# Optimization experiments

Hardware: AMD Instinct MI355X
Metric: run time of the kernel (lower is better)

Reference implementation:

```python
import jax, jax.numpy as jnp
import numpy as np

OUT = 7   # output_size
SR = 2    # sampling_ratio


def _roi_align(feat_bhwc, rois, batch_idx, sx, sy):
    """RoIAlign (torchvision semantics, aligned=False) with per-axis spatial scale.
    feat_bhwc: [B,H,W,C]; rois: [K,4] (x1,y1,x2,y2) in padded-image coords;
    batch_idx: [K] int32; returns [K,C,OUT,OUT]."""
    B, H, W, C = feat_bhwc.shape
    K = rois.shape[0]
    x1 = rois[:, 0] * sx
    y1 = rois[:, 1] * sy
    x2 = rois[:, 2] * sx
    y2 = rois[:, 3] * sy
    bw = jnp.maximum(x2 - x1, 1.0) / OUT   # bin width  [K]
    bh = jnp.maximum(y2 - y1, 1.0) / OUT   # bin height [K]
    # sample position j in [0, OUT*SR): offset (j+0.5)/SR bins from roi start
    g = (jnp.arange(OUT * SR, dtype=feat_bhwc.dtype) + 0.5) / SR
    ys = y1[:, None] + g[None, :] * bh[:, None]   # [K, P] with P = OUT*SR
    xs = x1[:, None] + g[None, :] * bw[:, None]   # [K, P]
    Y = ys[:, :, None]                            # [K,P,1]
    X = xs[:, None, :]                            # [K,1,P]
    valid = (Y >= -1.0) & (Y <= H) & (X >= -1.0) & (X <= W)  # [K,P,P]
    Yc = jnp.clip(Y, 0.0, H - 1)
    Xc = jnp.clip(X, 0.0, W - 1)
    y0f = jnp.floor(Yc)
    x0f = jnp.floor(Xc)
    ly = Yc - y0f
    lx = Xc - x0f
    hy = 1.0 - ly
    hx = 1.0 - lx
    y0i = y0f.astype(jnp.int32)
    x0i = x0f.astype(jnp.int32)
    y1i = jnp.minimum(y0i + 1, H - 1)
    x1i = jnp.minimum(x0i + 1, W - 1)
    b = batch_idx[:, None, None]                  # [K,1,1]

    def gat(yi, xi):
        # broadcasts indices to [K,P,P]; gathers [K,P,P,C]
        return feat_bhwc[b, yi, xi]

    out = ((hy * hx)[..., None] * gat(y0i, x0i)
           + (hy * lx)[..., None] * gat(y0i, x1i)
           + (ly * hx)[..., None] * gat(y1i, x0i)
           + (ly * lx)[..., None] * gat(y1i, x1i))
    out = out * valid[..., None].astype(out.dtype)
    # average SRxSR samples per output bin
    out = out.reshape(K, OUT, SR, OUT, SR, C).mean(axis=(2, 4))
    return out.transpose(0, 3, 1, 2)  # [K,C,OUT,OUT]


def reference(x0, x1, x2, boxes, ratio, offset, shape):
    B, C0, H0, W0 = x0.shape
    # bilinear upsample (half-pixel centers == torch align_corners=False) and concat
    up1 = jax.image.resize(x1, (B, x1.shape[1], H0, W0), method='bilinear')
    up2 = jax.image.resize(x2, (B, x2.shape[1], H0, W0), method='bilinear')
    feat = jnp.concatenate([x0, up1, up2], axis=1)      # [B, 3*C, H0, W0]
    feat_bhwc = feat.transpose(0, 2, 3, 1)
    # map boxes from original-image coords to padded/resized coords
    rH, rW = ratio[:, 0], ratio[:, 1]
    top, left = offset[:, 0], offset[:, 1]
    mul = jnp.stack([rW, rH, rW, rH], axis=-1)[:, None, :]   # [B,1,4]
    add = jnp.stack([left, top, left, top], axis=-1)[:, None, :]
    rois = (boxes * mul + add).reshape(-1, 4)                # [K,4]
    N = boxes.shape[1]
    batch_idx = jnp.repeat(jnp.arange(B, dtype=jnp.int32), N)
    # per-axis spatial scale from the first meta (as in the torch code)
    padded_h = jnp.floor(shape[0, 0] * rH[0] + 2.0 * top[0])
    padded_w = jnp.floor(shape[0, 1] * rW[0] + 2.0 * left[0])
    sx = W0 / padded_w
    sy = H0 / padded_h
    return _roi_align(feat_bhwc, rois, batch_idx, sx, sy)   # [B*N, 3*C, 7, 7]


def setup_inputs():
    key = jax.random.key(0)
    k = jax.random.split(key, 5)
    B, C, N = 2, 256, 128
    IH, IW = 800.0, 1216.0  # original image size; stride-8 top level -> 100x152
    x0 = jax.random.normal(k[0], (B, C, 100, 152), jnp.float32)
    x1 = jax.random.normal(k[1], (B, C, 50, 76), jnp.float32)
    x2 = jax.random.normal(k[2], (B, C, 25, 38), jnp.float32)
    xy = jax.random.uniform(k[3], (B, N, 2)) * jnp.array([IW - 64.0, IH - 64.0], jnp.float32)
    wh = 16.0 + jax.random.uniform(k[4], (B, N, 2)) * 200.0
    boxes = jnp.concatenate([xy, jnp.minimum(xy + wh, jnp.array([IW, IH], jnp.float32))], axis=-1)
    ratio = jnp.ones((B, 2), jnp.float32)
    offset = jnp.zeros((B, 2), jnp.float32)
    shape = jnp.tile(jnp.array([[IH, IW]], jnp.float32), (B, 1))
    return dict(x0=x0, x1=x1, x2=x2, boxes=boxes, ratio=ratio, offset=offset, shape=shape)
```

## Files before the change

### kernel.cpp

```cpp
#include <hip/hip_runtime.h>
#include <hip/hip_bf16.h>

constexpr int B  = 2;
constexpr int C  = 256;
constexpr int H0 = 100, W0 = 152;
constexpr int H1 = 50,  W1 = 76;
constexpr int H2 = 25,  W2 = 38;
constexpr int N  = 128;
constexpr int K  = B * N;
constexpr int CT = 3 * C;
constexpr int OUTS = 7;

#define DEV __device__ __forceinline__

DEV float ldbf(const __hip_bfloat16* p) { return __bfloat162float(*p); }

DEV void st4bf(__hip_bfloat16* p, float a, float b, float c, float d) {
  union { __hip_bfloat16 h[4]; uint2 u; } pk;
  pk.h[0] = __float2bfloat16(a); pk.h[1] = __float2bfloat16(b);
  pk.h[2] = __float2bfloat16(c); pk.h[3] = __float2bfloat16(d);
  *reinterpret_cast<uint2*>(p) = pk.u;
}

__global__ __launch_bounds__(256) void fuse_kernel(
    const float* __restrict__ x0, const float* __restrict__ x1,
    const float* __restrict__ x2, __hip_bfloat16* __restrict__ feat) {
  __shared__ float buf[64 * 153];
  const int blk  = blockIdx.x;
  const int tile = blk % 12;
  const int by   = blk / 12;
  const int y    = by % H0;
  const int b    = by / H0;
  const int t    = threadIdx.x;
  const int level = tile >> 2;
  const int c0l   = (tile & 3) * 64;

  __hip_bfloat16* const orow =
      feat + (((size_t)b * H0 + y) * W0) * CT + tile * 64;

  if (level == 0) {
    const float* src = x0 + (((size_t)b * C + c0l) * H0 + y) * W0;
    for (int i = 0; i < 10; ++i) {
      const int lin = i * 256 + t;
      if (lin < 2432) {
        const int cl = lin / 38, xq = lin % 38;
        const float4 v =
            *reinterpret_cast<const float4*>(src + (size_t)cl * (H0 * W0) + xq * 4);
        float* d = &buf[cl * 153 + xq * 4];
        d[0] = v.x; d[1] = v.y; d[2] = v.z; d[3] = v.w;
      }
    }
    __syncthreads();
    for (int i = 0; i < 10; ++i) {
      const int lin = i * 256 + t;
      if (lin < 2432) {
        const int x = lin >> 4, cq = lin & 15;
        st4bf(orow + (size_t)x * CT + cq * 4,
              buf[(cq * 4 + 0) * 153 + x], buf[(cq * 4 + 1) * 153 + x],
              buf[(cq * 4 + 2) * 153 + x], buf[(cq * 4 + 3) * 153 + x]);
      }
    }
  } else if (level == 1) {
    const float fy = fminf(fmaxf(y * 0.5f - 0.25f, 0.f), (float)(H1 - 1));
    const int   y0i = (int)fy;
    const float ly  = fy - (float)y0i;
    const int   y1i = min(y0i + 1, H1 - 1);
    const int rstep = (y1i - y0i) * W1;
    const float* s0 = x1 + (((size_t)b * C + c0l) * H1 + y0i) * W1;
    for (int i = 0; i < 5; ++i) {
      const int lin = i * 256 + t;
      if (lin < 1216) {
        const int cl = lin / 19, xq = lin % 19;
        const float* p = s0 + (size_t)cl * (H1 * W1) + xq * 4;
        const float4 v0 = *reinterpret_cast<const float4*>(p);
        const float4 v1 = *reinterpret_cast<const float4*>(p + rstep);
        float* d = &buf[cl * 81 + xq * 4];
        d[0] = v0.x + ly * (v1.x - v0.x);
        d[1] = v0.y + ly * (v1.y - v0.y);
        d[2] = v0.z + ly * (v1.z - v0.z);
        d[3] = v0.w + ly * (v1.w - v0.w);
      }
    }
    __syncthreads();
    for (int i = 0; i < 10; ++i) {
      const int lin = i * 256 + t;
      if (lin < 2432) {
        const int x = lin >> 4, cq = lin & 15;
        const float fx = fminf(fmaxf(x * 0.5f - 0.25f, 0.f), (float)(W1 - 1));
        const int   x0i = (int)fx;
        const float lx  = fx - (float)x0i;
        const int   x1i = min(x0i + 1, W1 - 1);
        const float* r = &buf[cq * 4 * 81];
        float v[4];
        #pragma unroll
        for (int j = 0; j < 4; ++j) {
          const float a = r[j * 81 + x0i], bb = r[j * 81 + x1i];
          v[j] = a + lx * (bb - a);
        }
        st4bf(orow + (size_t)x * CT + cq * 4, v[0], v[1], v[2], v[3]);
      }
    }
  } else {
    const float fy = fminf(fmaxf(y * 0.25f - 0.375f, 0.f), (float)(H2 - 1));
    const int   y0i = (int)fy;
    const float ly  = fy - (float)y0i;
    const int   y1i = min(y0i + 1, H2 - 1);
    const int rstep = (y1i - y0i) * W2;
    const float* s0 = x2 + (((size_t)b * C + c0l) * H2 + y0i) * W2;
    for (int i = 0; i < 5; ++i) {
      const int lin = i * 256 + t;
      if (lin < 1216) {
        const int cl = lin / 19, xq = lin % 19;
        const float* p = s0 + (size_t)cl * (H2 * W2) + xq * 2;
        const float2 v0 = *reinterpret_cast<const float2*>(p);
        const float2 v1 = *reinterpret_cast<const float2*>(p + rstep);
        float* d = &buf[cl * 39 + xq * 2];
        d[0] = v0.x + ly * (v1.x - v0.x);
        d[1] = v0.y + ly * (v1.y - v0.y);
      }
    }
    __syncthreads();
    for (int i = 0; i < 10; ++i) {
      const int lin = i * 256 + t;
      if (lin < 2432) {
        const int x = lin >> 4, cq = lin & 15;
        const float fx = fminf(fmaxf(x * 0.25f - 0.375f, 0.f), (float)(W2 - 1));
        const int   x0i = (int)fx;
        const float lx  = fx - (float)x0i;
        const int   x1i = min(x0i + 1, W2 - 1);
        const float* r = &buf[cq * 4 * 39];
        float v[4];
        #pragma unroll
        for (int j = 0; j < 4; ++j) {
          const float a = r[j * 39 + x0i], bb = r[j * 39 + x1i];
          v[j] = a + lx * (bb - a);
        }
        st4bf(orow + (size_t)x * CT + cq * 4, v[0], v[1], v[2], v[3]);
      }
    }
  }
}

__global__ __launch_bounds__(256, 3) void roi_kernel(
    const __hip_bfloat16* __restrict__ feat, const float* __restrict__ boxes,
    const float* __restrict__ ratio, const float* __restrict__ offset,
    const float* __restrict__ shape, float* __restrict__ out) {
  __shared__ float lds[256 * 49];
  const int blk = blockIdx.x;
  const int cg  = blk % 3;
  const int k   = blk / 3;
  const int b   = k >> 7;
  const int t   = threadIdx.x;
  const int c   = cg * 256 + t;

  const float padded_h = floorf(shape[0] * ratio[0] + 2.f * offset[0]);
  const float padded_w = floorf(shape[1] * ratio[1] + 2.f * offset[1]);
  const float sx = (float)W0 / padded_w;
  const float sy = (float)H0 / padded_h;
  const float rHb = ratio[b * 2 + 0], rWb = ratio[b * 2 + 1];
  const float topb = offset[b * 2 + 0], leftb = offset[b * 2 + 1];
  const float* bx = boxes + (size_t)k * 4;
  const float x1s = (bx[0] * rWb + leftb) * sx;
  const float y1s = (bx[1] * rHb + topb) * sy;
  const float x2s = (bx[2] * rWb + leftb) * sx;
  const float y2s = (bx[3] * rHb + topb) * sy;
  const float bw = fmaxf(x2s - x1s, 1.f) / OUTS;
  const float bh = fmaxf(y2s - y1s, 1.f) / OUTS;

  float hx[14], lx[14];
  int xo0[14], xo1[14];
  #pragma unroll
  for (int s = 0; s < 14; ++s) {
    const float X = x1s + ((float)s * 0.5f + 0.25f) * bw;
    const bool vx = (X >= -1.f) && (X <= (float)W0);
    const float Xc = fminf(fmaxf(X, 0.f), (float)(W0 - 1));
    const float xf = floorf(Xc);
    const float l  = Xc - xf;
    const int x0i = (int)xf;
    const int x1i = min(x0i + 1, W0 - 1);
    hx[s]  = vx ? (1.f - l) : 0.f;
    lx[s]  = vx ? l : 0.f;
    xo0[s] = x0i * CT;
    xo1[s] = x1i * CT;
  }

  const __hip_bfloat16* fb = feat + (size_t)b * (H0 * W0 * CT) + c;

  for (int ph = 0; ph < OUTS; ++ph) {
    float acc[OUTS] = {0.f, 0.f, 0.f, 0.f, 0.f, 0.f, 0.f};
    #pragma unroll
    for (int iy = 0; iy < 2; ++iy) {
      const float Y = y1s + ((float)ph + (float)iy * 0.5f + 0.25f) * bh;
      const bool vy = (Y >= -1.f) && (Y <= (float)H0);
      const float Yc = fminf(fmaxf(Y, 0.f), (float)(H0 - 1));
      const float yf = floorf(Yc);
      const float ly = Yc - yf;
      const int y0i = (int)yf;
      const int y1i = min(y0i + 1, H0 - 1);
      const float w0 = vy ? (1.f - ly) * 0.25f : 0.f;
      const float w1 = vy ? ly * 0.25f : 0.f;
      const __hip_bfloat16* r0 = fb + (size_t)y0i * (W0 * CT);
      const __hip_bfloat16* r1 = fb + (size_t)y1i * (W0 * CT);
      float v00[14], v01[14], v10[14], v11[14];
      #pragma unroll
      for (int s = 0; s < 14; ++s) {
        v00[s] = ldbf(r0 + xo0[s]);
        v01[s] = ldbf(r0 + xo1[s]);
        v10[s] = ldbf(r1 + xo0[s]);
        v11[s] = ldbf(r1 + xo1[s]);
      }
      #pragma unroll
      for (int s = 0; s < 14; ++s) {
        acc[s >> 1] += w0 * (hx[s] * v00[s] + lx[s] * v01[s]) +
                       w1 * (hx[s] * v10[s] + lx[s] * v11[s]);
      }
    }
    #pragma unroll
    for (int pw = 0; pw < OUTS; ++pw) lds[t * 49 + ph * 7 + pw] = acc[pw];
  }
  __syncthreads();
  float* ob = out + (size_t)k * (CT * 49) + (size_t)cg * (256 * 49);
  const float4* ls = reinterpret_cast<const float4*>(lds);
  float4* os = reinterpret_cast<float4*>(ob);
  for (int i = 0; i < 13; ++i) {
    const int idx = i * 256 + t;
    if (idx < 3136) os[idx] = ls[idx];
  }
}

extern "C" void kernel_launch(void* const* d_in, const int* in_sizes, int n_in,
                              void* d_out, int out_size, void* d_ws, size_t ws_size,
                              hipStream_t stream) {
  const float* x0     = (const float*)d_in[0];
  const float* x1     = (const float*)d_in[1];
  const float* x2     = (const float*)d_in[2];
  const float* boxes  = (const float*)d_in[3];
  const float* ratio  = (const float*)d_in[4];
  const float* offset = (const float*)d_in[5];
  const float* shape  = (const float*)d_in[6];
  float* out = (float*)d_out;

  __hip_bfloat16* feat = (__hip_bfloat16*)d_ws;
  const dim3 blk(256);
  const dim3 g1(B * H0 * 12);
  const dim3 g2(K * 3);

  fuse_kernel<<<g1, blk, 0, stream>>>(x0, x1, x2, feat);
  roi_kernel<<<g2, blk, 0, stream>>>(feat, boxes, ratio, offset, shape, out);
}
```

Before: 140.0 us.

## Fold upsampling into RoIAlign by composing bilinear weights over low-res levels

```diff
diff --git a/kernel.cpp b/kernel.cpp
--- a/kernel.cpp
+++ b/kernel.cpp
@@ -8,8 +8,11 @@
 constexpr int H2 = 25,  W2 = 38;
 constexpr int N  = 128;
 constexpr int K  = B * N;
-constexpr int CT = 3 * C;
 constexpr int OUTS = 7;
+
+constexpr size_t F0E = (size_t)B * H0 * W0 * C;
+constexpr size_t F1E = (size_t)B * H1 * W1 * C;
+constexpr size_t F2E = (size_t)B * H2 * W2 * C;
 
 #define DEV __device__ __forceinline__
 
@@ -22,136 +25,105 @@
   *reinterpret_cast<uint2*>(p) = pk.u;
 }
 
-__global__ __launch_bounds__(256) void fuse_kernel(
+__global__ __launch_bounds__(256) void transpose_kernel(
     const float* __restrict__ x0, const float* __restrict__ x1,
-    const float* __restrict__ x2, __hip_bfloat16* __restrict__ feat) {
+    const float* __restrict__ x2, __hip_bfloat16* __restrict__ f0,
+    __hip_bfloat16* __restrict__ f1, __hip_bfloat16* __restrict__ f2) {
   __shared__ float buf[64 * 153];
-  const int blk  = blockIdx.x;
-  const int tile = blk % 12;
-  const int by   = blk / 12;
-  const int y    = by % H0;
-  const int b    = by / H0;
-  const int t    = threadIdx.x;
-  const int level = tile >> 2;
-  const int c0l   = (tile & 3) * 64;
-
-  __hip_bfloat16* const orow =
-      feat + (((size_t)b * H0 + y) * W0) * CT + tile * 64;
-
-  if (level == 0) {
+  const int blk = blockIdx.x;
+  const int t   = threadIdx.x;
+
+  if (blk < 800) {
+    const int tile = blk & 3, y = (blk >> 2) % H0, b = blk / 400;
+    const int c0l = tile * 64;
     const float* src = x0 + (((size_t)b * C + c0l) * H0 + y) * W0;
     for (int i = 0; i < 10; ++i) {
       const int lin = i * 256 + t;
-      if (lin < 2432) {
+      if (lin < 64 * 38) {
         const int cl = lin / 38, xq = lin % 38;
-        const float4 v =
-            *reinterpret_cast<const float4*>(src + (size_t)cl * (H0 * W0) + xq * 4);
+        const float4 v = *reinterpret_cast<const float4*>(
+            src + (size_t)cl * (H0 * W0) + xq * 4);
         float* d = &buf[cl * 153 + xq * 4];
         d[0] = v.x; d[1] = v.y; d[2] = v.z; d[3] = v.w;
       }
     }
     __syncthreads();
+    __hip_bfloat16* dst = f0 + (((size_t)b * H0 + y) * W0) * C + c0l;
     for (int i = 0; i < 10; ++i) {
       const int lin = i * 256 + t;
-      if (lin < 2432) {
+      if (lin < W0 * 16) {
         const int x = lin >> 4, cq = lin & 15;
-        st4bf(orow + (size_t)x * CT + cq * 4,
+        st4bf(dst + (size_t)x * C + cq * 4,
               buf[(cq * 4 + 0) * 153 + x], buf[(cq * 4 + 1) * 153 + x],
               buf[(cq * 4 + 2) * 153 + x], buf[(cq * 4 + 3) * 153 + x]);
       }
     }
-  } else if (level == 1) {
-    const float fy = fminf(fmaxf(y * 0.5f - 0.25f, 0.f), (float)(H1 - 1));
-    const int   y0i = (int)fy;
-    const float ly  = fy - (float)y0i;
-    const int   y1i = min(y0i + 1, H1 - 1);
-    const int rstep = (y1i - y0i) * W1;
-    const float* s0 = x1 + (((size_t)b * C + c0l) * H1 + y0i) * W1;
+  } else if (blk < 1200) {
+    const int j = blk - 800;
+    const int tile = j & 3, y = (j >> 2) % H1, b = j / 200;
+    const int c0l = tile * 64;
+    const float* src = x1 + (((size_t)b * C + c0l) * H1 + y) * W1;
     for (int i = 0; i < 5; ++i) {
       const int lin = i * 256 + t;
-      if (lin < 1216) {
+      if (lin < 64 * 19) {
         const int cl = lin / 19, xq = lin % 19;
-        const float* p = s0 + (size_t)cl * (H1 * W1) + xq * 4;
-        const float4 v0 = *reinterpret_cast<const float4*>(p);
-        const float4 v1 = *reinterpret_cast<const float4*>(p + rstep);
-        float* d = &buf[cl * 81 + xq * 4];
-        d[0] = v0.x + ly * (v1.x - v0.x);
-        d[1] = v0.y + ly * (v1.y - v0.y);
-        d[2] = v0.z + ly * (v1.z - v0.z);
-        d[3] = v0.w + ly * (v1.w - v0.w);
+        const float4 v = *reinterpret_cast<const float4*>(
+            src + (size_t)cl * (H1 * W1) + xq * 4);
+        float* d = &buf[cl * 77 + xq * 4];
+        d[0] = v.x; d[1] = v.y; d[2] = v.z; d[3] = v.w;
       }
     }
     __syncthreads();
-    for (int i = 0; i < 10; ++i) {
-      const int lin = i * 256 + t;
-      if (lin < 2432) {
+    __hip_bfloat16* dst = f1 + (((size_t)b * H1 + y) * W1) * C + c0l;
+    for (int i = 0; i < 5; ++i) {
+      const int lin = i * 256 + t;
+      if (lin < W1 * 16) {
         const int x = lin >> 4, cq = lin & 15;
-        const float fx = fminf(fmaxf(x * 0.5f - 0.25f, 0.f), (float)(W1 - 1));
-        const int   x0i = (int)fx;
-        const float lx  = fx - (float)x0i;
-        const int   x1i = min(x0i + 1, W1 - 1);
-        const float* r = &buf[cq * 4 * 81];
-        float v[4];
-        #pragma unroll
-        for (int j = 0; j < 4; ++j) {
-          const float a = r[j * 81 + x0i], bb = r[j * 81 + x1i];
-          v[j] = a + lx * (bb - a);
-        }
-        st4bf(orow + (size_t)x * CT + cq * 4, v[0], v[1], v[2], v[3]);
+        st4bf(dst + (size_t)x * C + cq * 4,
+              buf[(cq * 4 + 0) * 77 + x], buf[(cq * 4 + 1) * 77 + x],
+              buf[(cq * 4 + 2) * 77 + x], buf[(cq * 4 + 3) * 77 + x]);
       }
     }
   } else {
-    const float fy = fminf(fmaxf(y * 0.25f - 0.375f, 0.f), (float)(H2 - 1));
-    const int   y0i = (int)fy;
-    const float ly  = fy - (float)y0i;
-    const int   y1i = min(y0i + 1, H2 - 1);
-    const int rstep = (y1i - y0i) * W2;
-    const float* s0 = x2 + (((size_t)b * C + c0l) * H2 + y0i) * W2;
+    const int j = blk - 1200;
+    const int tile = j & 3, y = (j >> 2) % H2, b = j / 100;
+    const int c0l = tile * 64;
+    const float* src = x2 + (((size_t)b * C + c0l) * H2 + y) * W2;
     for (int i = 0; i < 5; ++i) {
       const int lin = i * 256 + t;
-      if (lin < 1216) {
+      if (lin < 64 * 19) {
         const int cl = lin / 19, xq = lin % 19;
-        const float* p = s0 + (size_t)cl * (H2 * W2) + xq * 2;
-        const float2 v0 = *reinterpret_cast<const float2*>(p);
-        const float2 v1 = *reinterpret_cast<const float2*>(p + rstep);
+        const float2 v = *reinterpret_cast<const float2*>(
+            src + (size_t)cl * (H2 * W2) + xq * 2);
         float* d = &buf[cl * 39 + xq * 2];
-        d[0] = v0.x + ly * (v1.x - v0.x);
-        d[1] = v0.y + ly * (v1.y - v0.y);
+        d[0] = v.x; d[1] = v.y;
       }
     }
     __syncthreads();
-    for (int i = 0; i < 10; ++i) {
-      const int lin = i * 256 + t;
-      if (lin < 2432) {
+    __hip_bfloat16* dst = f2 + (((size_t)b * H2 + y) * W2) * C + c0l;
+    for (int i = 0; i < 3; ++i) {
+      const int lin = i * 256 + t;
+      if (lin < W2 * 16) {
         const int x = lin >> 4, cq = lin & 15;
-        const float fx = fminf(fmaxf(x * 0.25f - 0.375f, 0.f), (float)(W2 - 1));
-        const int   x0i = (int)fx;
-        const float lx  = fx - (float)x0i;
-        const int   x1i = min(x0i + 1, W2 - 1);
-        const float* r = &buf[cq * 4 * 39];
-        float v[4];
-        #pragma unroll
-        for (int j = 0; j < 4; ++j) {
-          const float a = r[j * 39 + x0i], bb = r[j * 39 + x1i];
-          v[j] = a + lx * (bb - a);
-        }
-        st4bf(orow + (size_t)x * CT + cq * 4, v[0], v[1], v[2], v[3]);
+        st4bf(dst + (size_t)x * C + cq * 4,
+              buf[(cq * 4 + 0) * 39 + x], buf[(cq * 4 + 1) * 39 + x],
+              buf[(cq * 4 + 2) * 39 + x], buf[(cq * 4 + 3) * 39 + x]);
       }
     }
   }
 }
 
 __global__ __launch_bounds__(256, 3) void roi_kernel(
-    const __hip_bfloat16* __restrict__ feat, const float* __restrict__ boxes,
+    const __hip_bfloat16* __restrict__ f0, const __hip_bfloat16* __restrict__ f1,
+    const __hip_bfloat16* __restrict__ f2, const float* __restrict__ boxes,
     const float* __restrict__ ratio, const float* __restrict__ offset,
     const float* __restrict__ shape, float* __restrict__ out) {
   __shared__ float lds[256 * 49];
   const int blk = blockIdx.x;
-  const int cg  = blk % 3;
+  const int lvl = blk % 3;
   const int k   = blk / 3;
   const int b   = k >> 7;
   const int t   = threadIdx.x;
-  const int c   = cg * 256 + t;
 
   const float padded_h = floorf(shape[0] * ratio[0] + 2.f * offset[0]);
   const float padded_w = floorf(shape[1] * ratio[1] + 2.f * offset[1]);
@@ -167,59 +139,134 @@
   const float bw = fmaxf(x2s - x1s, 1.f) / OUTS;
   const float bh = fmaxf(y2s - y1s, 1.f) / OUTS;
 
-  float hx[14], lx[14];
-  int xo0[14], xo1[14];
-  #pragma unroll
-  for (int s = 0; s < 14; ++s) {
-    const float X = x1s + ((float)s * 0.5f + 0.25f) * bw;
-    const bool vx = (X >= -1.f) && (X <= (float)W0);
-    const float Xc = fminf(fmaxf(X, 0.f), (float)(W0 - 1));
-    const float xf = floorf(Xc);
-    const float l  = Xc - xf;
-    const int x0i = (int)xf;
-    const int x1i = min(x0i + 1, W0 - 1);
-    hx[s]  = vx ? (1.f - l) : 0.f;
-    lx[s]  = vx ? l : 0.f;
-    xo0[s] = x0i * CT;
-    xo1[s] = x1i * CT;
-  }
-
-  const __hip_bfloat16* fb = feat + (size_t)b * (H0 * W0 * CT) + c;
-
-  for (int ph = 0; ph < OUTS; ++ph) {
-    float acc[OUTS] = {0.f, 0.f, 0.f, 0.f, 0.f, 0.f, 0.f};
+  if (lvl == 0) {
+    float hx[14], lx[14];
+    int xo0[14], xo1[14];
     #pragma unroll
-    for (int iy = 0; iy < 2; ++iy) {
-      const float Y = y1s + ((float)ph + (float)iy * 0.5f + 0.25f) * bh;
-      const bool vy = (Y >= -1.f) && (Y <= (float)H0);
-      const float Yc = fminf(fmaxf(Y, 0.f), (float)(H0 - 1));
-      const float yf = floorf(Yc);
-      const float ly = Yc - yf;
-      const int y0i = (int)yf;
-      const int y1i = min(y0i + 1, H0 - 1);
-      const float w0 = vy ? (1.f - ly) * 0.25f : 0.f;
-      const float w1 = vy ? ly * 0.25f : 0.f;
-      const __hip_bfloat16* r0 = fb + (size_t)y0i * (W0 * CT);
-      const __hip_bfloat16* r1 = fb + (size_t)y1i * (W0 * CT);
-      float v00[14], v01[14], v10[14], v11[14];
-      #pragma unroll
-      for (int s = 0; s < 14; ++s) {
-        v00[s] = ldbf(r0 + xo0[s]);
-        v01[s] = ldbf(r0 + xo1[s]);
-        v10[s] = ldbf(r1 + xo0[s]);
-        v11[s] = ldbf(r1 + xo1[s]);
-      }
-      #pragma unroll
-      for (int s = 0; s < 14; ++s) {
-        acc[s >> 1] += w0 * (hx[s] * v00[s] + lx[s] * v01[s]) +
-                       w1 * (hx[s] * v10[s] + lx[s] * v11[s]);
-      }
-    }
+    for (int s = 0; s < 14; ++s) {
+      const float X = x1s + ((float)s * 0.5f + 0.25f) * bw;
+      const bool vx = (X >= -1.f) && (X <= (float)W0);
+      const float Xc = fminf(fmaxf(X, 0.f), (float)(W0 - 1));
+      const float xf = floorf(Xc);
+      const float l  = Xc - xf;
+      const int x0i = (int)xf;
+      const int x1i = min(x0i + 1, W0 - 1);
+      hx[s]  = vx ? (1.f - l) : 0.f;
+      lx[s]  = vx ? l : 0.f;
+      xo0[s] = x0i * C;
+      xo1[s] = x1i * C;
+    }
+    const __hip_bfloat16* fb = f0 + (size_t)b * (H0 * W0 * C) + t;
+    for (int ph = 0; ph < OUTS; ++ph) {
+      float acc[OUTS] = {0.f, 0.f, 0.f, 0.f, 0.f, 0.f, 0.f};
+      #pragma unroll
+      for (int iy = 0; iy < 2; ++iy) {
+        const float Y = y1s + ((float)ph + (float)iy * 0.5f + 0.25f) * bh;
+        const bool vy = (Y >= -1.f) && (Y <= (float)H0);
+        const float Yc = fminf(fmaxf(Y, 0.f), (float)(H0 - 1));
+        const float yf = floorf(Yc);
+        const float ly = Yc - yf;
+        const int y0i = (int)yf;
+        const int y1i = min(y0i + 1, H0 - 1);
+        const float w0 = vy ? (1.f - ly) * 0.25f : 0.f;
+        const float w1 = vy ? ly * 0.25f : 0.f;
+        const __hip_bfloat16* r0 = fb + (size_t)y0i * (W0 * C);
+        const __hip_bfloat16* r1 = fb + (size_t)y1i * (W0 * C);
+        float v00[14], v01[14], v10[14], v11[14];
+        #pragma unroll
+        for (int s = 0; s < 14; ++s) {
+          v00[s] = ldbf(r0 + xo0[s]);
+          v01[s] = ldbf(r0 + xo1[s]);
+          v10[s] = ldbf(r1 + xo0[s]);
+          v11[s] = ldbf(r1 + xo1[s]);
+        }
+        #pragma unroll
+        for (int s = 0; s < 14; ++s) {
+          acc[s >> 1] += w0 * (hx[s] * v00[s] + lx[s] * v01[s]) +
+                         w1 * (hx[s] * v10[s] + lx[s] * v11[s]);
+        }
+      }
+      #pragma unroll
+      for (int pw = 0; pw < OUTS; ++pw) lds[t * 49 + ph * 7 + pw] = acc[pw];
+    }
+  } else {
+    const float sc = (lvl == 1) ? 0.5f : 0.25f;
+    const float of = (lvl == 1) ? -0.25f : -0.375f;
+    const int  Hl = (lvl == 1) ? H1 : H2;
+    const int  Wl = (lvl == 1) ? W1 : W2;
+    const __hip_bfloat16* fsrc =
+        ((lvl == 1) ? f1 : f2) + (size_t)b * ((size_t)Hl * Wl * C) + t;
+
+    int co0[14], co1[14], co2[14];
+    float cw0[14], cw1[14], cw2[14];
     #pragma unroll
-    for (int pw = 0; pw < OUTS; ++pw) lds[t * 49 + ph * 7 + pw] = acc[pw];
+    for (int s = 0; s < 14; ++s) {
+      const float X = x1s + ((float)s * 0.5f + 0.25f) * bw;
+      const bool vx = (X >= -1.f) && (X <= (float)W0);
+      const float Xc = fminf(fmaxf(X, 0.f), (float)(W0 - 1));
+      const float xf = floorf(Xc);
+      const float fr = Xc - xf;
+      const int xa = (int)xf;
+      const int xb = min(xa + 1, W0 - 1);
+      const float hw = vx ? (1.f - fr) : 0.f;
+      const float lw = vx ? fr : 0.f;
+      const float sa = fminf(fmaxf((float)xa * sc + of, 0.f), (float)(Wl - 1));
+      const float sb = fminf(fmaxf((float)xb * sc + of, 0.f), (float)(Wl - 1));
+      const int qa = (int)sa; const float fa = sa - (float)qa;
+      const int qb = (int)sb; const float fb2 = sb - (float)qb;
+      const int d = qb - qa;
+      cw0[s] = hw * (1.f - fa) + ((d == 0) ? lw * (1.f - fb2) : 0.f);
+      cw1[s] = hw * fa + ((d == 0) ? lw * fb2 : lw * (1.f - fb2));
+      cw2[s] = (d == 1) ? lw * fb2 : 0.f;
+      co0[s] = qa * C;
+      co1[s] = min(qa + 1, Wl - 1) * C;
+      co2[s] = min(qa + 2, Wl - 1) * C;
+    }
+
+    for (int ph = 0; ph < OUTS; ++ph) {
+      float acc[OUTS] = {0.f, 0.f, 0.f, 0.f, 0.f, 0.f, 0.f};
+      #pragma unroll
+      for (int iy = 0; iy < 2; ++iy) {
+        const float Y = y1s + ((float)ph + (float)iy * 0.5f + 0.25f) * bh;
+        const bool vy = (Y >= -1.f) && (Y <= (float)H0);
+        const float Yc = fminf(fmaxf(Y, 0.f), (float)(H0 - 1));
+        const float yf = floorf(Yc);
+        const float fr = Yc - yf;
+        const int ya = (int)yf;
+        const int yb = min(ya + 1, H0 - 1);
+        const float Aw = vy ? (1.f - fr) * 0.25f : 0.f;
+        const float Bw = vy ? fr * 0.25f : 0.f;
+        const float ta = fminf(fmaxf((float)ya * sc + of, 0.f), (float)(Hl - 1));
+        const float tb = fminf(fmaxf((float)yb * sc + of, 0.f), (float)(Hl - 1));
+        const int ra = (int)ta; const float ga = ta - (float)ra;
+        const int rb = (int)tb; const float gb = tb - (float)rb;
+        const int e = rb - ra;
+        const float rw0 = Aw * (1.f - ga) + ((e == 0) ? Bw * (1.f - gb) : 0.f);
+        const float rw1 = Aw * ga + ((e == 0) ? Bw * gb : Bw * (1.f - gb));
+        const float rw2 = (e == 1) ? Bw * gb : 0.f;
+        const __hip_bfloat16* p0 = fsrc + (size_t)ra * (Wl * C);
+        const __hip_bfloat16* p1 = fsrc + (size_t)min(ra + 1, Hl - 1) * (Wl * C);
+        const __hip_bfloat16* p2 = fsrc + (size_t)min(ra + 2, Hl - 1) * (Wl * C);
+        #pragma unroll
+        for (int s = 0; s < 14; ++s) {
+          const float r0v = cw0[s] * ldbf(p0 + co0[s]) +
+                            cw1[s] * ldbf(p0 + co1[s]) +
+                            cw2[s] * ldbf(p0 + co2[s]);
+          const float r1v = cw0[s] * ldbf(p1 + co0[s]) +
+                            cw1[s] * ldbf(p1 + co1[s]) +
+                            cw2[s] * ldbf(p1 + co2[s]);
+          const float r2v = cw0[s] * ldbf(p2 + co0[s]) +
+                            cw1[s] * ldbf(p2 + co1[s]) +
+                            cw2[s] * ldbf(p2 + co2[s]);
+          acc[s >> 1] += rw0 * r0v + rw1 * r1v + rw2 * r2v;
+        }
+      }
+      #pragma unroll
+      for (int pw = 0; pw < OUTS; ++pw) lds[t * 49 + ph * 7 + pw] = acc[pw];
+    }
   }
   __syncthreads();
-  float* ob = out + (size_t)k * (CT * 49) + (size_t)cg * (256 * 49);
+  float* ob = out + (size_t)k * (768 * 49) + (size_t)lvl * (256 * 49);
   const float4* ls = reinterpret_cast<const float4*>(lds);
   float4* os = reinterpret_cast<float4*>(ob);
   for (int i = 0; i < 13; ++i) {
@@ -240,11 +287,12 @@
   const float* shape  = (const float*)d_in[6];
   float* out = (float*)d_out;
 
-  __hip_bfloat16* feat = (__hip_bfloat16*)d_ws;
+  __hip_bfloat16* f0 = (__hip_bfloat16*)d_ws;
+  __hip_bfloat16* f1 = f0 + F0E;
+  __hip_bfloat16* f2 = f1 + F1E;
+
   const dim3 blk(256);
-  const dim3 g1(B * H0 * 12);
-  const dim3 g2(K * 3);
-
-  fuse_kernel<<<g1, blk, 0, stream>>>(x0, x1, x2, feat);
-  roi_kernel<<<g2, blk, 0, stream>>>(feat, boxes, ratio, offset, shape, out);
-}
+  transpose_kernel<<<dim3(1400), blk, 0, stream>>>(x0, x1, x2, f0, f1, f2);
+  roi_kernel<<<dim3(K * 3), blk, 0, stream>>>(f0, f1, f2, boxes, ratio,
+                                              offset, shape, out);
+}
```

Measured after the change: 197.2 us. 1.41x slower.
